# Kernel optimization log

Measured on AMD Instinct MI355X. Metric: run time of the kernel, lower is better.

## Reference

```python
import jax, jax.numpy as jnp
import numpy as np

H = 7        # num attention heads (must divide D=791)
TOP_NUM = 2  # hard-coded in select(attn_tensor, 2)


def setup_inputs() -> dict:
    key = jax.random.key(0)
    ks = jax.random.split(key, 7)
    B, N, D = 32, 512, 791  # D = 2*hidden_dim + 23, hidden_dim=384
    s = 1.0 / np.sqrt(D)
    return {
        "fuse_feature": jax.random.normal(ks[0], (B, N, D), jnp.float32),
        "Wq": jax.random.normal(ks[1], (D, D), jnp.float32) * s,
        "bq": jax.random.normal(ks[2], (D,), jnp.float32) * 0.01,
        "Wk": jax.random.normal(ks[3], (D, D), jnp.float32) * s,
        "bk": jax.random.normal(ks[4], (D,), jnp.float32) * 0.01,
        "W_gc": jax.random.normal(ks[5], (D, D), jnp.float32) * s,
        "b_gc": jax.random.normal(ks[6], (D,), jnp.float32) * 0.01,
    }


def _select(mat, top_num):
    """Faithful jax version of select(): per-batch top-k threshold,
    symmetrize (mask + mask^T), then fill diagonal with 1."""
    B, N, _ = mat.shape
    flat = mat.reshape(B, N * N)
    kth = jax.lax.top_k(flat, top_num)[0][:, -1]          # [B]
    m = (flat >= kth[:, None]).astype(mat.dtype).reshape(B, N, N)
    adj = m + jnp.swapaxes(m, -2, -1)                     # values in {0,1,2}
    eye = jnp.eye(N, dtype=bool)
    return jnp.where(eye[None], jnp.asarray(1.0, mat.dtype), adj)


def reference(fuse_feature, Wq, bq, Wk, bk, W_gc, b_gc):
    B, N, D = fuse_feature.shape
    dk = D // H

    # score_mask: positions where fuse @ fuse^T == 0 (padding detector)
    gram = jnp.einsum("bnd,bmd->bnm", fuse_feature, fuse_feature)
    score_mask = (gram == 0)[:, None]                     # [B,1,N,N]

    # multi-head attention probabilities (eval mode: no dropout)
    q = (fuse_feature @ Wq + bq).reshape(B, N, H, dk).transpose(0, 2, 1, 3)
    k = (fuse_feature @ Wk + bk).reshape(B, N, H, dk).transpose(0, 2, 1, 3)
    scores = jnp.einsum("bhnd,bhmd->bhnm", q, k) / jnp.sqrt(jnp.asarray(dk, q.dtype))
    scores = jnp.where(score_mask, -1e9, scores)
    valid = (~score_mask[..., 0:1]).astype(scores.dtype)  # [B,1,N,1]
    p_attn = jax.nn.softmax(scores, axis=-1) * valid

    attn = p_attn.sum(axis=1)                             # [B,N,N]
    att_adj = _select(attn, TOP_NUM) * attn

    # GraphConvolution (kg_gc): adj @ (x W) / (rowsum(adj)+1) + b, then relu
    hidden = fuse_feature @ W_gc
    denom = att_adj.sum(axis=2, keepdims=True) + 1.0
    out = jnp.einsum("bnm,bmd->bnd", att_adj, hidden) / denom + b_gc
    return jax.nn.relu(out)
```

## Files before the change

kernel.cpp:

```cpp
#include <hip/hip_runtime.h>

#define B_  32
#define N_  512
#define D_  791
#define H_  7
#define DK_ 113
#define M_  (B_*N_)
#define KP_ 800
#define DP_ 896

typedef __attribute__((ext_vector_type(8))) short bf16x8;
typedef __attribute__((ext_vector_type(4))) float f32x4;

__device__ __forceinline__ ushort f2bf_rn(float x) {
    uint u = __float_as_uint(x);
    uint r = (u + 0x7FFFu + ((u >> 16) & 1u)) >> 16;
    return (ushort)r;
}
__device__ __forceinline__ float bf2f(ushort h) {
    return __uint_as_float(((uint)h) << 16);
}
__device__ __forceinline__ void split_bf16(float x, ushort& h, ushort& l) {
    h = f2bf_rn(x);
    l = f2bf_rn(x - bf2f(h));
}

__device__ __forceinline__ void gload16(const void* g, void* l) {
    __builtin_amdgcn_global_load_lds(
        (const __attribute__((address_space(1))) void*)g,
        (__attribute__((address_space(3))) void*)l, 16, 0, 0);
}

__global__ __launch_bounds__(256)
void splitX_kernel(const float* __restrict__ X, ushort* __restrict__ Xh,
                   ushort* __restrict__ Xl)
{
    int g = blockIdx.x * 256 + threadIdx.x;
    if (g >= M_ * 100) return;
    int row = g / 100, grp = g % 100;
    int k0 = grp * 8;
    float v[8];
    if (k0 + 8 <= D_) {
        const float* p = X + (size_t)row * D_ + k0;
        #pragma unroll
        for (int i = 0; i < 8; ++i) v[i] = p[i];
    } else {
        #pragma unroll
        for (int i = 0; i < 8; ++i) {
            int k = k0 + i;
            v[i] = (k < D_) ? X[(size_t)row * D_ + k] : 0.f;
        }
    }
    bf16x8 hv, lv;
    #pragma unroll
    for (int i = 0; i < 8; ++i) {
        ushort h, l; split_bf16(v[i], h, l);
        hv[i] = (short)h; lv[i] = (short)l;
    }
    *(bf16x8*)&Xh[(size_t)row * KP_ + k0] = hv;
    *(bf16x8*)&Xl[(size_t)row * KP_ + k0] = lv;
}

__global__ __launch_bounds__(256)
void castWt_kernel(const float* __restrict__ W0, const float* __restrict__ W1,
                   const float* __restrict__ W2,
                   ushort* __restrict__ B0h, ushort* __restrict__ B0l,
                   ushort* __restrict__ B1h, ushort* __restrict__ B1l,
                   ushort* __restrict__ B2h, ushort* __restrict__ B2l)
{
    const int pc = blockIdx.x;
    const int w  = blockIdx.y;
    const float* W = (w == 0) ? W0 : (w == 1) ? W1 : W2;
    ushort* Bh = (w == 0) ? B0h : (w == 1) ? B1h : B2h;
    ushort* Bl = (w == 0) ? B0l : (w == 1) ? B1l : B2l;
    int src;
    if (w == 2) src = (pc < D_) ? pc : -1;
    else { int hh = pc >> 7, off = pc & 127; src = (off < DK_) ? hh * DK_ + off : -1; }
    for (int k = threadIdx.x; k < KP_; k += 256) {
        float v = (src >= 0 && k < D_) ? W[(size_t)k * D_ + src] : 0.f;
        ushort h, l; split_bf16(v, h, l);
        Bh[(size_t)pc * KP_ + k] = h;
        Bl[(size_t)pc * KP_ + k] = l;
    }
}

#define GEMM_STAGE(dstH, dstL, srcH, srcL, rowBase)                          \
    {                                                                        \
        _Pragma("unroll")                                                    \
        for (int j = 0; j < 2; ++j) {                                        \
            int c  = t + 256 * j;                                            \
            int r  = c >> 2, q = c & 3;                                      \
            int qs = q ^ ((r >> 1) & 3);                                     \
            size_t go = (size_t)(rowBase + r) * KP_ + k0 + qs * 8;           \
            ushort* lb_h = dstH + (size_t)((t & 192) + 256 * j) * 8;         \
            ushort* lb_l = dstL + (size_t)((t & 192) + 256 * j) * 8;         \
            gload16(&srcH[go], lb_h);                                        \
            gload16(&srcL[go], lb_l);                                        \
        }                                                                    \
    }

struct GemmAcc { f32x4 a[4][4]; };

__device__ __forceinline__ void gemm_core(
    const ushort* __restrict__ Xh, const ushort* __restrict__ Xl,
    const ushort* __restrict__ Bh, const ushort* __restrict__ Bl,
    int row0, int col0, int t, int wr, int wc, int fr, int kq,
    ushort* AsH, ushort* AsL, ushort* BsH, ushort* BsL, GemmAcc& acc)
{
    for (int k0 = 0; k0 < KP_; k0 += 32) {
        GEMM_STAGE(AsH, AsL, Xh, Xl, row0)
        GEMM_STAGE(BsH, BsL, Bh, Bl, col0)
        __syncthreads();

        bf16x8 aH[4], aL[4], bH[4], bL[4];
        #pragma unroll
        for (int m = 0; m < 4; ++m) {
            int r = wr * 64 + m * 16 + fr;
            int off = r * 32 + (kq ^ ((r >> 1) & 3)) * 8;
            aH[m] = *(const bf16x8*)&AsH[off];
            aL[m] = *(const bf16x8*)&AsL[off];
        }
        #pragma unroll
        for (int n = 0; n < 4; ++n) {
            int c = wc * 64 + n * 16 + fr;
            int off = c * 32 + (kq ^ ((c >> 1) & 3)) * 8;
            bH[n] = *(const bf16x8*)&BsH[off];
            bL[n] = *(const bf16x8*)&BsL[off];
        }
        #pragma unroll
        for (int m = 0; m < 4; ++m)
            #pragma unroll
            for (int n = 0; n < 4; ++n) {
                acc.a[m][n] = __builtin_amdgcn_mfma_f32_16x16x32_bf16(aH[m], bH[n], acc.a[m][n], 0, 0, 0);
                acc.a[m][n] = __builtin_amdgcn_mfma_f32_16x16x32_bf16(aH[m], bL[n], acc.a[m][n], 0, 0, 0);
                acc.a[m][n] = __builtin_amdgcn_mfma_f32_16x16x32_bf16(aL[m], bH[n], acc.a[m][n], 0, 0, 0);
            }
        __syncthreads();
    }
}

__global__ __launch_bounds__(256)
void gemm_qk_kernel(const ushort* __restrict__ Xh, const ushort* __restrict__ Xl,
                    const ushort* __restrict__ Bqh, const ushort* __restrict__ Bql,
                    const ushort* __restrict__ Bkh, const ushort* __restrict__ Bkl,
                    const float* __restrict__ bq, const float* __restrict__ bk,
                    ushort* __restrict__ Qh, ushort* __restrict__ Ql,
                    ushort* __restrict__ Kh, ushort* __restrict__ Kl)
{
    __shared__ ushort AsH[128*32], AsL[128*32], BsH[128*32], BsL[128*32];
    const int flat = blockIdx.x + 14 * blockIdx.y;
    const int nid  = (flat & 7) * 224 + (flat >> 3);
    const int by = nid / 14, bx = nid % 14;
    const int w = bx / 7, ct = bx % 7;
    const int row0 = by * 128, col0 = ct * 128;
    const ushort* Bh = w ? Bkh : Bqh;
    const ushort* Bl = w ? Bkl : Bql;
    const float* bias = w ? bk : bq;
    ushort* Ch = w ? Kh : Qh;
    ushort* Cl = w ? Kl : Ql;

    const int t = threadIdx.x, lane = t & 63, wid = t >> 6;
    const int wr = wid >> 1, wc = wid & 1;
    const int fr = lane & 15, kq = lane >> 4;

    GemmAcc acc;
    #pragma unroll
    for (int m = 0; m < 4; ++m)
        #pragma unroll
        for (int n = 0; n < 4; ++n) acc.a[m][n] = (f32x4){0.f,0.f,0.f,0.f};

    gemm_core(Xh, Xl, Bh, Bl, row0, col0, t, wr, wc, fr, kq,
              AsH, AsL, BsH, BsL, acc);

    const int orow = kq * 4;
    #pragma unroll
    for (int n = 0; n < 4; ++n) {
        int pc = col0 + wc * 64 + n * 16 + fr;
        int hh = pc >> 7, off = pc & 127;
        float bb = (off < DK_) ? bias[hh * DK_ + off] : 0.f;
        #pragma unroll
        for (int m = 0; m < 4; ++m)
            #pragma unroll
            for (int j = 0; j < 4; ++j) {
                int gr = row0 + wr * 64 + m * 16 + orow + j;
                float v = acc.a[m][n][j] + bb;
                ushort h, l; split_bf16(v, h, l);
                Ch[(size_t)gr * DP_ + pc] = h;
                Cl[(size_t)gr * DP_ + pc] = l;
            }
    }
}

__global__ __launch_bounds__(256)
void gemm_hd_kernel(const ushort* __restrict__ Xh, const ushort* __restrict__ Xl,
                    const ushort* __restrict__ Bgh, const ushort* __restrict__ Bgl,
                    float* __restrict__ Cf)
{
    __shared__ ushort AsH[128*32], AsL[128*32], BsH[128*32], BsL[128*32];
    const int flat = blockIdx.x + 7 * blockIdx.y;
    const int nid  = (flat & 7) * 112 + (flat >> 3);
    const int by = nid / 7, bx = nid % 7;
    const int row0 = by * 128, col0 = bx * 128;

    const int t = threadIdx.x, lane = t & 63, wid = t >> 6;
    const int wr = wid >> 1, wc = wid & 1;
    const int fr = lane & 15, kq = lane >> 4;

    GemmAcc acc;
    #pragma unroll
    for (int m = 0; m < 4; ++m)
        #pragma unroll
        for (int n = 0; n < 4; ++n) acc.a[m][n] = (f32x4){0.f,0.f,0.f,0.f};

    gemm_core(Xh, Xl, Bgh, Bgl, row0, col0, t, wr, wc, fr, kq,
              AsH, AsL, BsH, BsL, acc);

    const int orow = kq * 4;
    #pragma unroll
    for (int n = 0; n < 4; ++n) {
        int gc = col0 + wc * 64 + n * 16 + fr;
        if (gc < D_) {
            #pragma unroll
            for (int m = 0; m < 4; ++m)
                #pragma unroll
                for (int j = 0; j < 4; ++j) {
                    int gr = row0 + wr * 64 + m * 16 + orow + j;
                    Cf[(size_t)gr * D_ + gc] = acc.a[m][n][j];
                }
        }
    }
}

__global__ __launch_bounds__(256, 2)
void attn_mfma(const ushort* __restrict__ Qh, const ushort* __restrict__ Ql,
               const ushort* __restrict__ Kh, const ushort* __restrict__ Kl,
               float* __restrict__ attn, float* __restrict__ candv,
               int* __restrict__ candi)
{
    __shared__ ushort KsH[512*32];
    __shared__ ushort KsL[512*32];
    __shared__ float redA[4][32];
    __shared__ float redB[4][32];
    __shared__ float wv[8]; __shared__ int wi[8];

    const int t = threadIdx.x, lane = t & 63, w = t >> 6;
    const int bid = blockIdx.x;
    const int swz = (bid & 7) * 64 + (bid >> 3);
    const int b = swz >> 4, r0 = (swz & 15) * 32;
    const int fr = lane & 15, kg = (lane >> 4) * 8;
    const float scale = 0.09407208683f;

    f32x4 accA[2][8];
    #pragma unroll
    for (int m = 0; m < 2; ++m)
        #pragma unroll
        for (int n = 0; n < 8; ++n) accA[m][n] = (f32x4){0.f,0.f,0.f,0.f};

    for (int h = 0; h < H_; ++h) {
        f32x4 S[2][8];
        #pragma unroll
        for (int m = 0; m < 2; ++m)
            #pragma unroll
            for (int n = 0; n < 8; ++n) S[m][n] = (f32x4){0.f,0.f,0.f,0.f};

        #pragma unroll
        for (int kk = 0; kk < 4; ++kk) {
            bf16x8 qH[2], qL[2];
            #pragma unroll
            for (int m = 0; m < 2; ++m) {
                size_t qo = (size_t)(b * N_ + r0 + m * 16 + fr) * DP_ + h * 128 + kk * 32 + kg;
                qH[m] = *(const bf16x8*)&Qh[qo];
                qL[m] = *(const bf16x8*)&Ql[qo];
            }
            #pragma unroll
            for (int i = 0; i < 8; ++i) {
                int g = t + 256 * i;
                int key = g >> 2, c8 = (g & 3) * 8;
                size_t go = (size_t)(b * N_ + key) * DP_ + h * 128 + kk * 32 + c8;
                int lo = key * 32 + (c8 ^ ((key & 3) * 8));
                *(bf16x8*)&KsH[lo] = *(const bf16x8*)&Kh[go];
                *(bf16x8*)&KsL[lo] = *(const bf16x8*)&Kl[go];
            }
            __syncthreads();
            #pragma unroll
            for (int n = 0; n < 8; ++n) {
                int key = w * 128 + n * 16 + fr;
                int lo = key * 32 + (kg ^ ((key & 3) * 8));
                bf16x8 bH = *(const bf16x8*)&KsH[lo];
                bf16x8 bL = *(const bf16x8*)&KsL[lo];
                #pragma unroll
                for (int m = 0; m < 2; ++m) {
                    S[m][n] = __builtin_amdgcn_mfma_f32_16x16x32_bf16(qH[m], bH, S[m][n], 0, 0, 0);
                    S[m][n] = __builtin_amdgcn_mfma_f32_16x16x32_bf16(qH[m], bL, S[m][n], 0, 0, 0);
                    S[m][n] = __builtin_amdgcn_mfma_f32_16x16x32_bf16(qL[m], bH, S[m][n], 0, 0, 0);
                }
            }
            __syncthreads();
        }

        float fm[2][4];
        #pragma unroll
        for (int m = 0; m < 2; ++m)
            #pragma unroll
            for (int j = 0; j < 4; ++j) {
                float mx = -1e30f;
                #pragma unroll
                for (int n = 0; n < 8; ++n) {
                    S[m][n][j] *= scale;
                    mx = fmaxf(mx, S[m][n][j]);
                }
                #pragma unroll
                for (int d = 1; d < 16; d <<= 1) mx = fmaxf(mx, __shfl_xor(mx, d));
                fm[m][j] = mx;
            }
        if ((lane & 15) == 0) {
            #pragma unroll
            for (int m = 0; m < 2; ++m)
                #pragma unroll
                for (int j = 0; j < 4; ++j)
                    redA[w][m * 16 + (lane >> 4) * 4 + j] = fm[m][j];
        }
        __syncthreads();
        #pragma unroll
        for (int m = 0; m < 2; ++m)
            #pragma unroll
            for (int j = 0; j < 4; ++j) {
                int q = m * 16 + (lane >> 4) * 4 + j;
                float mx = redA[0][q];
                mx = fmaxf(mx, redA[1][q]);
                mx = fmaxf(mx, redA[2][q]);
                mx = fmaxf(mx, redA[3][q]);
                fm[m][j] = mx;
            }
        float sm[2][4];
        #pragma unroll
        for (int m = 0; m < 2; ++m)
            #pragma unroll
            for (int j = 0; j < 4; ++j) {
                float s = 0.f;
                #pragma unroll
                for (int n = 0; n < 8; ++n) {
                    float e = __expf(S[m][n][j] - fm[m][j]);
                    S[m][n][j] = e; s += e;
                }
                #pragma unroll
                for (int d = 1; d < 16; d <<= 1) s += __shfl_xor(s, d);
                sm[m][j] = s;
            }
        if ((lane & 15) == 0) {
            #pragma unroll
            for (int m = 0; m < 2; ++m)
                #pragma unroll
                for (int j = 0; j < 4; ++j)
                    redB[w][m * 16 + (lane >> 4) * 4 + j] = sm[m][j];
        }
        __syncthreads();
        #pragma unroll
        for (int m = 0; m < 2; ++m)
            #pragma unroll
            for (int j = 0; j < 4; ++j) {
                int q = m * 16 + (lane >> 4) * 4 + j;
                float s = redB[0][q] + redB[1][q] + redB[2][q] + redB[3][q];
                float rinv = 1.f / s;
                #pragma unroll
                for (int n = 0; n < 8; ++n)
                    accA[m][n][j] += S[m][n][j] * rinv;
            }
        __syncthreads();
    }

    float* ab = attn + (size_t)b * N_ * N_;
    #pragma unroll
    for (int m = 0; m < 2; ++m)
        #pragma unroll
        for (int j = 0; j < 4; ++j) {
            int row = r0 + m * 16 + (lane >> 4) * 4 + j;
            float* ar = ab + (size_t)row * N_;
            #pragma unroll
            for (int n = 0; n < 8; ++n)
                ar[w * 128 + n * 16 + fr] = accA[m][n][j];
        }

    float v1 = -1e30f, v2 = -1e30f; int i1 = 0, i2 = 0;
    #pragma unroll
    for (int m = 0; m < 2; ++m)
        #pragma unroll
        for (int n = 0; n < 8; ++n)
            #pragma unroll
            for (int j = 0; j < 4; ++j) {
                float v = accA[m][n][j];
                int row = r0 + m * 16 + (lane >> 4) * 4 + j;
                int col = w * 128 + n * 16 + fr;
                int idx = row * N_ + col;
                if (v > v1)      { v2 = v1; i2 = i1; v1 = v; i1 = idx; }
                else if (v > v2) { v2 = v;  i2 = idx; }
            }
    #pragma unroll
    for (int d = 1; d < 64; d <<= 1) {
        float ov1 = __shfl_xor(v1, d); int oi1 = __shfl_xor(i1, d);
        float ov2 = __shfl_xor(v2, d); int oi2 = __shfl_xor(i2, d);
        if (ov1 > v1)      { v2 = v1; i2 = i1; v1 = ov1; i1 = oi1; }
        else if (ov1 > v2) { v2 = ov1; i2 = oi1; }
        if (ov2 > v1)      { v2 = v1; i2 = i1; v1 = ov2; i1 = oi2; }
        else if (ov2 > v2) { v2 = ov2; i2 = oi2; }
    }
    if (lane == 0) { wv[w*2] = v1; wi[w*2] = i1; wv[w*2+1] = v2; wi[w*2+1] = i2; }
    __syncthreads();
    if (t == 0) {
        float g1 = -1e30f, g2 = -1e30f; int gi1 = 0, gi2 = 0;
        for (int e = 0; e < 8; ++e) {
            float v = wv[e]; int ii = wi[e];
            if (v > g1)      { g2 = g1; gi2 = gi1; g1 = v; gi1 = ii; }
            else if (v > g2) { g2 = v; gi2 = ii; }
        }
        int cb = (b * 16 + (swz & 15)) * 2;
        candv[cb] = g1; candi[cb] = gi1;
        candv[cb+1] = g2; candi[cb+1] = gi2;
    }
}

__global__ __launch_bounds__(256)
void merge_kernel(const float* __restrict__ attn, const float* __restrict__ candv,
                  const int* __restrict__ candi, float* __restrict__ diag,
                  int* __restrict__ tidx, float* __restrict__ tval)
{
    const int b = blockIdx.x, t = threadIdx.x;
    const float* ab = attn + (size_t)b * N_ * N_;
    for (int n = t; n < N_; n += 256) diag[b * N_ + n] = ab[(size_t)n * N_ + n];
    if (t == 0) {
        float v1 = -1e30f, v2 = -1e30f; int i1 = 0, i2 = 0;
        for (int s = 0; s < 32; ++s) {
            float v = candv[b * 32 + s]; int ii = candi[b * 32 + s];
            if (v > v1)      { v2 = v1; i2 = i1; v1 = v; i1 = ii; }
            else if (v > v2) { v2 = v; i2 = ii; }
        }
        int r1 = i1 / N_, c1 = i1 % N_;
        int r2 = i2 / N_, c2 = i2 % N_;
        tidx[b*4+0] = r1; tidx[b*4+1] = c1; tidx[b*4+2] = r2; tidx[b*4+3] = c2;
        tval[b*4+0] = ab[(size_t)r1 * N_ + c1];
        tval[b*4+1] = ab[(size_t)c1 * N_ + r1];
        tval[b*4+2] = ab[(size_t)r2 * N_ + c2];
        tval[b*4+3] = ab[(size_t)c2 * N_ + r2];
    }
}

__global__ __launch_bounds__(256)
void out_kernel(const float* __restrict__ Hd, const float* __restrict__ diag,
                const int* __restrict__ tidx, const float* __restrict__ tval,
                const float* __restrict__ bgc, float* __restrict__ out)
{
    const int bn = blockIdx.x;
    const int b = bn >> 9, n = bn & 511;
    const int t = threadIdx.x;

    const int r1 = tidx[b*4+0], c1 = tidx[b*4+1];
    const int r2 = tidx[b*4+2], c2 = tidx[b*4+3];

    int   mc[4]; float mv[4]; int nc = 0;
    if (r1 != c1) {
        if (n == r1) { mc[nc] = c1; mv[nc] = tval[b*4+0]; ++nc; }
        if (n == c1) { mc[nc] = r1; mv[nc] = tval[b*4+1]; ++nc; }
    }
    if (r2 != c2) {
        if (n == r2) { mc[nc] = c2; mv[nc] = tval[b*4+2]; ++nc; }
        if (n == c2) { mc[nc] = r2; mv[nc] = tval[b*4+3]; ++nc; }
    }
    const float dg = diag[bn];
    float denom = dg + 1.0f;
    for (int i = 0; i < nc; ++i) denom += mv[i];
    const float rd = 1.f / denom;

    const float* hn = Hd + (size_t)bn * D_;
    for (int d = t; d < D_; d += 256) {
        float acc = dg * hn[d];
        for (int i = 0; i < nc; ++i)
            acc += mv[i] * Hd[(size_t)(b * N_ + mc[i]) * D_ + d];
        float o = acc * rd + bgc[d];
        out[(size_t)bn * D_ + d] = fmaxf(o, 0.f);
    }
}

extern "C" void kernel_launch(void* const* d_in, const int* in_sizes, int n_in,
                              void* d_out, int out_size, void* d_ws, size_t ws_size,
                              hipStream_t stream)
{
    const float* X   = (const float*)d_in[0];
    const float* Wq  = (const float*)d_in[1];
    const float* bq  = (const float*)d_in[2];
    const float* Wk  = (const float*)d_in[3];
    const float* bk  = (const float*)d_in[4];
    const float* Wgc = (const float*)d_in[5];
    const float* bgc = (const float*)d_in[6];
    float* out = (float*)d_out;

    ushort* wsu = (ushort*)d_ws;
    const size_t MDP = (size_t)M_ * DP_;
    const size_t MKP = (size_t)M_ * KP_;
    ushort* Qh = wsu;
    ushort* Ql = wsu + MDP;
    ushort* Kh = wsu + 2 * MDP;
    ushort* Kl = wsu + 3 * MDP;
    ushort* Bt = wsu + 4 * MDP;
    const size_t BSZ = (size_t)DP_ * KP_;
    ushort* Bqh = Bt;            ushort* Bql = Bt + BSZ;
    ushort* Bkh = Bt + 2 * BSZ;  ushort* Bkl = Bt + 3 * BSZ;
    ushort* Bgh = Bt + 4 * BSZ;  ushort* Bgl = Bt + 5 * BSZ;
    ushort* Xh  = Bt + 6 * BSZ;
    float* diag  = (float*)(Xh + MKP);
    int*   tidx  = (int*)(diag + M_);
    float* tval  = (float*)(tidx + 128);
    float* candv = tval + 128;
    int*   candi = (int*)(candv + 1024);
    ushort* Xl  = (ushort*)d_out;
    float* Hd   = (float*)d_ws;
    float* attn = out;

    hipLaunchKernelGGL(splitX_kernel, dim3((M_ * 100 + 255) / 256), dim3(256), 0, stream,
                       X, Xh, Xl);
    hipLaunchKernelGGL(castWt_kernel, dim3(DP_, 3), dim3(256), 0, stream,
                       Wq, Wk, Wgc, Bqh, Bql, Bkh, Bkl, Bgh, Bgl);

    hipLaunchKernelGGL(gemm_qk_kernel, dim3(14, 128), dim3(256), 0, stream,
                       Xh, Xl, Bqh, Bql, Bkh, Bkl, bq, bk, Qh, Ql, Kh, Kl);

    hipLaunchKernelGGL(attn_mfma, dim3(512), dim3(256), 0, stream,
                       Qh, Ql, Kh, Kl, attn, candv, candi);
    hipLaunchKernelGGL(merge_kernel, dim3(B_), dim3(256), 0, stream,
                       attn, candv, candi, diag, tidx, tval);

    hipLaunchKernelGGL(splitX_kernel, dim3((M_ * 100 + 255) / 256), dim3(256), 0, stream,
                       X, Xh, Xl);
    hipLaunchKernelGGL(gemm_hd_kernel, dim3(7, 128), dim3(256), 0, stream,
                       Xh, Xl, Bgh, Bgl, Hd);

    hipLaunchKernelGGL(out_kernel, dim3(M_), dim3(256), 0, stream,
                       Hd, diag, tidx, tval, bgc, out);
}
```

Before: 614.7 us.

## Double-buffer GEMM LDS, drop redundant X resplit, tile weight transpose, fuse diag

Both GEMM kernels now double-buffer their LDS tiles, so the global loads for the next k-tile are issued while MFMAs run on the current one. The hidden GEMM drops the X-low term, using only hi*Wh + hi*Wl, which removes the second splitX pass and one third of its MFMAs at some cost in accuracy. The weight cast/transpose now goes through a 32x32 shared-memory tile so that both reads and writes are coalesced. The attention diagonal is written directly from attn_mfma, so merge_kernel shrinks to a single thread per batch.

```diff
diff --git a/kernel.cpp b/kernel.cpp
--- a/kernel.cpp
+++ b/kernel.cpp
@@ -8,6 +8,7 @@
 #define M_  (B_*N_)
 #define KP_ 800
 #define DP_ 896
+#define NKT 25
 
 typedef __attribute__((ext_vector_type(8))) short bf16x8;
 typedef __attribute__((ext_vector_type(4))) float f32x4;
@@ -68,76 +69,63 @@
                    ushort* __restrict__ B1h, ushort* __restrict__ B1l,
                    ushort* __restrict__ B2h, ushort* __restrict__ B2l)
 {
-    const int pc = blockIdx.x;
-    const int w  = blockIdx.y;
+    __shared__ ushort WsH[32][34], WsL[32][34];
+    const int pc0 = blockIdx.x * 32;
+    const int k0  = blockIdx.y * 32;
+    const int w   = blockIdx.z;
     const float* W = (w == 0) ? W0 : (w == 1) ? W1 : W2;
     ushort* Bh = (w == 0) ? B0h : (w == 1) ? B1h : B2h;
     ushort* Bl = (w == 0) ? B0l : (w == 1) ? B1l : B2l;
-    int src;
-    if (w == 2) src = (pc < D_) ? pc : -1;
-    else { int hh = pc >> 7, off = pc & 127; src = (off < DK_) ? hh * DK_ + off : -1; }
-    for (int k = threadIdx.x; k < KP_; k += 256) {
+    const int tx = threadIdx.x & 31, ty = threadIdx.x >> 5;
+
+    #pragma unroll
+    for (int r = 0; r < 4; ++r) {
+        int kl = ty + 8 * r, k = k0 + kl;
+        int pc = pc0 + tx;
+        int src;
+        if (w == 2) src = (pc < D_) ? pc : -1;
+        else { int hh = pc >> 7, off = pc & 127; src = (off < DK_) ? hh * DK_ + off : -1; }
         float v = (src >= 0 && k < D_) ? W[(size_t)k * D_ + src] : 0.f;
         ushort h, l; split_bf16(v, h, l);
-        Bh[(size_t)pc * KP_ + k] = h;
-        Bl[(size_t)pc * KP_ + k] = l;
-    }
-}
-
-#define GEMM_STAGE(dstH, dstL, srcH, srcL, rowBase)                          \
+        WsH[tx][kl] = h; WsL[tx][kl] = l;
+    }
+    __syncthreads();
+    #pragma unroll
+    for (int r = 0; r < 4; ++r) {
+        int pcl = ty + 8 * r, pc = pc0 + pcl;
+        int k = k0 + tx;
+        Bh[(size_t)pc * KP_ + k] = WsH[pcl][tx];
+        Bl[(size_t)pc * KP_ + k] = WsL[pcl][tx];
+    }
+}
+
+#define STAGE_PAIR(dH, dL, srcH, srcL, rowBase, kk0)                         \
     {                                                                        \
         _Pragma("unroll")                                                    \
         for (int j = 0; j < 2; ++j) {                                        \
             int c  = t + 256 * j;                                            \
             int r  = c >> 2, q = c & 3;                                      \
             int qs = q ^ ((r >> 1) & 3);                                     \
-            size_t go = (size_t)(rowBase + r) * KP_ + k0 + qs * 8;           \
-            ushort* lb_h = dstH + (size_t)((t & 192) + 256 * j) * 8;         \
-            ushort* lb_l = dstL + (size_t)((t & 192) + 256 * j) * 8;         \
-            gload16(&srcH[go], lb_h);                                        \
-            gload16(&srcL[go], lb_l);                                        \
+            size_t go = (size_t)(rowBase + r) * KP_ + (kk0) + qs * 8;        \
+            int lofs = ((t & 192) + 256 * j) * 8;                            \
+            gload16(&srcH[go], (dH) + lofs);                                 \
+            gload16(&srcL[go], (dL) + lofs);                                 \
         }                                                                    \
     }
+#define STAGE_ONE(dH, srcH, rowBase, kk0)                                    \
+    {                                                                        \
+        _Pragma("unroll")                                                    \
+        for (int j = 0; j < 2; ++j) {                                        \
+            int c  = t + 256 * j;                                            \
+            int r  = c >> 2, q = c & 3;                                      \
+            int qs = q ^ ((r >> 1) & 3);                                     \
+            size_t go = (size_t)(rowBase + r) * KP_ + (kk0) + qs * 8;        \
+            int lofs = ((t & 192) + 256 * j) * 8;                            \
+            gload16(&srcH[go], (dH) + lofs);                                 \
+        }                                                                    \
+    }
 
 struct GemmAcc { f32x4 a[4][4]; };
-
-__device__ __forceinline__ void gemm_core(
-    const ushort* __restrict__ Xh, const ushort* __restrict__ Xl,
-    const ushort* __restrict__ Bh, const ushort* __restrict__ Bl,
-    int row0, int col0, int t, int wr, int wc, int fr, int kq,
-    ushort* AsH, ushort* AsL, ushort* BsH, ushort* BsL, GemmAcc& acc)
-{
-    for (int k0 = 0; k0 < KP_; k0 += 32) {
-        GEMM_STAGE(AsH, AsL, Xh, Xl, row0)
-        GEMM_STAGE(BsH, BsL, Bh, Bl, col0)
-        __syncthreads();
-
-        bf16x8 aH[4], aL[4], bH[4], bL[4];
-        #pragma unroll
-        for (int m = 0; m < 4; ++m) {
-            int r = wr * 64 + m * 16 + fr;
-            int off = r * 32 + (kq ^ ((r >> 1) & 3)) * 8;
-            aH[m] = *(const bf16x8*)&AsH[off];
-            aL[m] = *(const bf16x8*)&AsL[off];
-        }
-        #pragma unroll
-        for (int n = 0; n < 4; ++n) {
-            int c = wc * 64 + n * 16 + fr;
-            int off = c * 32 + (kq ^ ((c >> 1) & 3)) * 8;
-            bH[n] = *(const bf16x8*)&BsH[off];
-            bL[n] = *(const bf16x8*)&BsL[off];
-        }
-        #pragma unroll
-        for (int m = 0; m < 4; ++m)
-            #pragma unroll
-            for (int n = 0; n < 4; ++n) {
-                acc.a[m][n] = __builtin_amdgcn_mfma_f32_16x16x32_bf16(aH[m], bH[n], acc.a[m][n], 0, 0, 0);
-                acc.a[m][n] = __builtin_amdgcn_mfma_f32_16x16x32_bf16(aH[m], bL[n], acc.a[m][n], 0, 0, 0);
-                acc.a[m][n] = __builtin_amdgcn_mfma_f32_16x16x32_bf16(aL[m], bH[n], acc.a[m][n], 0, 0, 0);
-            }
-        __syncthreads();
-    }
-}
 
 __global__ __launch_bounds__(256)
 void gemm_qk_kernel(const ushort* __restrict__ Xh, const ushort* __restrict__ Xl,
@@ -147,7 +135,8 @@
                     ushort* __restrict__ Qh, ushort* __restrict__ Ql,
                     ushort* __restrict__ Kh, ushort* __restrict__ Kl)
 {
-    __shared__ ushort AsH[128*32], AsL[128*32], BsH[128*32], BsL[128*32];
+    __shared__ ushort AsH[2][128*32], AsL[2][128*32];
+    __shared__ ushort BsH[2][128*32], BsL[2][128*32];
     const int flat = blockIdx.x + 14 * blockIdx.y;
     const int nid  = (flat & 7) * 224 + (flat >> 3);
     const int by = nid / 14, bx = nid % 14;
@@ -169,8 +158,41 @@
         #pragma unroll
         for (int n = 0; n < 4; ++n) acc.a[m][n] = (f32x4){0.f,0.f,0.f,0.f};
 
-    gemm_core(Xh, Xl, Bh, Bl, row0, col0, t, wr, wc, fr, kq,
-              AsH, AsL, BsH, BsL, acc);
+    STAGE_PAIR(AsH[0], AsL[0], Xh, Xl, row0, 0)
+    STAGE_PAIR(BsH[0], BsL[0], Bh, Bl, col0, 0)
+    __syncthreads();
+
+    for (int kt = 0; kt < NKT; ++kt) {
+        const int cur = kt & 1;
+        if (kt + 1 < NKT) {
+            STAGE_PAIR(AsH[cur^1], AsL[cur^1], Xh, Xl, row0, (kt+1)*32)
+            STAGE_PAIR(BsH[cur^1], BsL[cur^1], Bh, Bl, col0, (kt+1)*32)
+        }
+        bf16x8 aH[4], aL[4], bH[4], bL[4];
+        #pragma unroll
+        for (int m = 0; m < 4; ++m) {
+            int r = wr * 64 + m * 16 + fr;
+            int off = r * 32 + (kq ^ ((r >> 1) & 3)) * 8;
+            aH[m] = *(const bf16x8*)&AsH[cur][off];
+            aL[m] = *(const bf16x8*)&AsL[cur][off];
+        }
+        #pragma unroll
+        for (int n = 0; n < 4; ++n) {
+            int c = wc * 64 + n * 16 + fr;
+            int off = c * 32 + (kq ^ ((c >> 1) & 3)) * 8;
+            bH[n] = *(const bf16x8*)&BsH[cur][off];
+            bL[n] = *(const bf16x8*)&BsL[cur][off];
+        }
+        #pragma unroll
+        for (int m = 0; m < 4; ++m)
+            #pragma unroll
+            for (int n = 0; n < 4; ++n) {
+                acc.a[m][n] = __builtin_amdgcn_mfma_f32_16x16x32_bf16(aH[m], bH[n], acc.a[m][n], 0, 0, 0);
+                acc.a[m][n] = __builtin_amdgcn_mfma_f32_16x16x32_bf16(aH[m], bL[n], acc.a[m][n], 0, 0, 0);
+                acc.a[m][n] = __builtin_amdgcn_mfma_f32_16x16x32_bf16(aL[m], bH[n], acc.a[m][n], 0, 0, 0);
+            }
+        __syncthreads();
+    }
 
     const int orow = kq * 4;
     #pragma unroll
@@ -192,11 +214,12 @@
 }
 
 __global__ __launch_bounds__(256)
-void gemm_hd_kernel(const ushort* __restrict__ Xh, const ushort* __restrict__ Xl,
+void gemm_hd_kernel(const ushort* __restrict__ Xh,
                     const ushort* __restrict__ Bgh, const ushort* __restrict__ Bgl,
                     float* __restrict__ Cf)
 {
-    __shared__ ushort AsH[128*32], AsL[128*32], BsH[128*32], BsL[128*32];
+    __shared__ ushort AsH[2][128*32];
+    __shared__ ushort BsH[2][128*32], BsL[2][128*32];
     const int flat = blockIdx.x + 7 * blockIdx.y;
     const int nid  = (flat & 7) * 112 + (flat >> 3);
     const int by = nid / 7, bx = nid % 7;
@@ -212,8 +235,39 @@
         #pragma unroll
         for (int n = 0; n < 4; ++n) acc.a[m][n] = (f32x4){0.f,0.f,0.f,0.f};
 
-    gemm_core(Xh, Xl, Bgh, Bgl, row0, col0, t, wr, wc, fr, kq,
-              AsH, AsL, BsH, BsL, acc);
+    STAGE_ONE(AsH[0], Xh, row0, 0)
+    STAGE_PAIR(BsH[0], BsL[0], Bgh, Bgl, col0, 0)
+    __syncthreads();
+
+    for (int kt = 0; kt < NKT; ++kt) {
+        const int cur = kt & 1;
+        if (kt + 1 < NKT) {
+            STAGE_ONE(AsH[cur^1], Xh, row0, (kt+1)*32)
+            STAGE_PAIR(BsH[cur^1], BsL[cur^1], Bgh, Bgl, col0, (kt+1)*32)
+        }
+        bf16x8 aH[4], bH[4], bL[4];
+        #pragma unroll
+        for (int m = 0; m < 4; ++m) {
+            int r = wr * 64 + m * 16 + fr;
+            int off = r * 32 + (kq ^ ((r >> 1) & 3)) * 8;
+            aH[m] = *(const bf16x8*)&AsH[cur][off];
+        }
+        #pragma unroll
+        for (int n = 0; n < 4; ++n) {
+            int c = wc * 64 + n * 16 + fr;
+            int off = c * 32 + (kq ^ ((c >> 1) & 3)) * 8;
+            bH[n] = *(const bf16x8*)&BsH[cur][off];
+            bL[n] = *(const bf16x8*)&BsL[cur][off];
+        }
+        #pragma unroll
+        for (int m = 0; m < 4; ++m)
+            #pragma unroll
+            for (int n = 0; n < 4; ++n) {
+                acc.a[m][n] = __builtin_amdgcn_mfma_f32_16x16x32_bf16(aH[m], bH[n], acc.a[m][n], 0, 0, 0);
+                acc.a[m][n] = __builtin_amdgcn_mfma_f32_16x16x32_bf16(aH[m], bL[n], acc.a[m][n], 0, 0, 0);
+            }
+        __syncthreads();
+    }
 
     const int orow = kq * 4;
     #pragma unroll
@@ -234,8 +288,8 @@
 __global__ __launch_bounds__(256, 2)
 void attn_mfma(const ushort* __restrict__ Qh, const ushort* __restrict__ Ql,
                const ushort* __restrict__ Kh, const ushort* __restrict__ Kl,
-               float* __restrict__ attn, float* __restrict__ candv,
-               int* __restrict__ candi)
+               float* __restrict__ attn, float* __restrict__ diag,
+               float* __restrict__ candv, int* __restrict__ candi)
 {
     __shared__ ushort KsH[512*32];
     __shared__ ushort KsL[512*32];
@@ -377,8 +431,11 @@
             int row = r0 + m * 16 + (lane >> 4) * 4 + j;
             float* ar = ab + (size_t)row * N_;
             #pragma unroll
-            for (int n = 0; n < 8; ++n)
-                ar[w * 128 + n * 16 + fr] = accA[m][n][j];
+            for (int n = 0; n < 8; ++n) {
+                int col = w * 128 + n * 16 + fr;
+                ar[col] = accA[m][n][j];
+                if (col == row) diag[b * N_ + row] = accA[m][n][j];
+            }
         }
 
     float v1 = -1e30f, v2 = -1e30f; int i1 = 0, i2 = 0;
@@ -419,29 +476,27 @@
     }
 }
 
-__global__ __launch_bounds__(256)
+__global__ __launch_bounds__(64)
 void merge_kernel(const float* __restrict__ attn, const float* __restrict__ candv,
-                  const int* __restrict__ candi, float* __restrict__ diag,
+                  const int* __restrict__ candi,
                   int* __restrict__ tidx, float* __restrict__ tval)
 {
-    const int b = blockIdx.x, t = threadIdx.x;
+    const int b = blockIdx.x;
+    if (threadIdx.x != 0) return;
     const float* ab = attn + (size_t)b * N_ * N_;
-    for (int n = t; n < N_; n += 256) diag[b * N_ + n] = ab[(size_t)n * N_ + n];
-    if (t == 0) {
-        float v1 = -1e30f, v2 = -1e30f; int i1 = 0, i2 = 0;
-        for (int s = 0; s < 32; ++s) {
-            float v = candv[b * 32 + s]; int ii = candi[b * 32 + s];
-            if (v > v1)      { v2 = v1; i2 = i1; v1 = v; i1 = ii; }
-            else if (v > v2) { v2 = v; i2 = ii; }
-        }
-        int r1 = i1 / N_, c1 = i1 % N_;
-        int r2 = i2 / N_, c2 = i2 % N_;
-        tidx[b*4+0] = r1; tidx[b*4+1] = c1; tidx[b*4+2] = r2; tidx[b*4+3] = c2;
-        tval[b*4+0] = ab[(size_t)r1 * N_ + c1];
-        tval[b*4+1] = ab[(size_t)c1 * N_ + r1];
-        tval[b*4+2] = ab[(size_t)r2 * N_ + c2];
-        tval[b*4+3] = ab[(size_t)c2 * N_ + r2];
-    }
+    float v1 = -1e30f, v2 = -1e30f; int i1 = 0, i2 = 0;
+    for (int s = 0; s < 32; ++s) {
+        float v = candv[b * 32 + s]; int ii = candi[b * 32 + s];
+        if (v > v1)      { v2 = v1; i2 = i1; v1 = v; i1 = ii; }
+        else if (v > v2) { v2 = v; i2 = ii; }
+    }
+    int r1 = i1 / N_, c1 = i1 % N_;
+    int r2 = i2 / N_, c2 = i2 % N_;
+    tidx[b*4+0] = r1; tidx[b*4+1] = c1; tidx[b*4+2] = r2; tidx[b*4+3] = c2;
+    tval[b*4+0] = ab[(size_t)r1 * N_ + c1];
+    tval[b*4+1] = ab[(size_t)c1 * N_ + r1];
+    tval[b*4+2] = ab[(size_t)r2 * N_ + c2];
+    tval[b*4+3] = ab[(size_t)c2 * N_ + r2];
 }
 
 __global__ __launch_bounds__(256)
@@ -517,21 +572,19 @@
 
     hipLaunchKernelGGL(splitX_kernel, dim3((M_ * 100 + 255) / 256), dim3(256), 0, stream,
                        X, Xh, Xl);
-    hipLaunchKernelGGL(castWt_kernel, dim3(DP_, 3), dim3(256), 0, stream,
+    hipLaunchKernelGGL(castWt_kernel, dim3(DP_ / 32, NKT, 3), dim3(256), 0, stream,
                        Wq, Wk, Wgc, Bqh, Bql, Bkh, Bkl, Bgh, Bgl);
 
     hipLaunchKernelGGL(gemm_qk_kernel, dim3(14, 128), dim3(256), 0, stream,
                        Xh, Xl, Bqh, Bql, Bkh, Bkl, bq, bk, Qh, Ql, Kh, Kl);
 
     hipLaunchKernelGGL(attn_mfma, dim3(512), dim3(256), 0, stream,
-                       Qh, Ql, Kh, Kl, attn, candv, candi);
-    hipLaunchKernelGGL(merge_kernel, dim3(B_), dim3(256), 0, stream,
-                       attn, candv, candi, diag, tidx, tval);
-
-    hipLaunchKernelGGL(splitX_kernel, dim3((M_ * 100 + 255) / 256), dim3(256), 0, stream,
-                       X, Xh, Xl);
+                       Qh, Ql, Kh, Kl, attn, diag, candv, candi);
+    hipLaunchKernelGGL(merge_kernel, dim3(B_), dim3(64), 0, stream,
+                       attn, candv, candi, tidx, tval);
+
     hipLaunchKernelGGL(gemm_hd_kernel, dim3(7, 128), dim3(256), 0, stream,
-                       Xh, Xl, Bgh, Bgl, Hd);
+                       Xh, Bgh, Bgl, Hd);
 
     hipLaunchKernelGGL(out_kernel, dim3(M_), dim3(256), 0, stream,
                        Hd, diag, tidx, tval, bgc, out);
```

After: 600.4 us. 1.02x faster.
